# Kernel optimization log

Measured on AMD Instinct MI355X. Metric: run time of the kernel, lower is better.

## Reference

```python
import jax, jax.numpy as jnp
import numpy as np

V = 163842  # icosphere level 7: 10*4^7 + 2
K = 6       # neighbors per vertex
G = 5       # gradient directions (conv kernel_size/stride)


def setup_inputs() -> dict:
    key = jax.random.key(0)
    k1, k2, k3, k4, k5 = jax.random.split(key, 5)
    N, C_in, C_out = 2, 32, 64
    x = jax.random.normal(k1, (N, C_in, V), dtype=jnp.float32)
    neighbor_idx = jax.random.randint(k2, (V, K), 0, V, dtype=jnp.int32)
    grad_w = jax.random.normal(k3, (V, G, K), dtype=jnp.float32) * 0.1
    conv_w = jax.random.normal(k4, (C_out, C_in, G), dtype=jnp.float32) * 0.05
    conv_b = jax.random.normal(k5, (C_out,), dtype=jnp.float32) * 0.01
    return {"x": x, "neighbor_idx": neighbor_idx, "grad_w": grad_w,
            "conv_w": conv_w, "conv_b": conv_b}


def reference(x, neighbor_idx, grad_w, conv_w, conv_b):
    # x: (N, C, V); neighbor_idx: (V, K); grad_w: (V, G, K)
    # 1) icosphere gradient: gather K neighbors per vertex, weighted sum -> (N, C, V, G)
    gathered = x[:, :, neighbor_idx]                       # (N, C, V, K)
    grads = jnp.einsum('ncvk,vgk->ncvg', gathered, grad_w)  # (N, C, V, G)
    # 2) Conv1d(kernel_size=5, stride=5) on (N, C, V*G) == per-vertex contraction over (c, g)
    out = jnp.einsum('ncvg,ocg->nov', grads, conv_w) + conv_b[None, :, None]
    return out  # (N, C_out, V)
```

## Files before the change

### kernel.cpp

```cpp
#include <hip/hip_runtime.h>
#include <hip/hip_bf16.h>

#define V_   163842
#define K_   6
#define G_   5
#define N_   2
#define CIN  32
#define COUT 64
#define CG   160
#define TV   64
#define CGP  168

typedef __attribute__((ext_vector_type(8))) short bf16x8;
typedef __attribute__((ext_vector_type(4))) float f32x4;
typedef __attribute__((ext_vector_type(2))) float f32x2;

__device__ __forceinline__ float bf2f(unsigned int u16) {
  union { unsigned int u; float f; } c; c.u = u16 << 16; return c.f;
}
__device__ __forceinline__ unsigned short f2bf(float f) {
  union { float f; unsigned int u; } c; c.f = f;
  unsigned int r = c.u + 0x7fffu + ((c.u >> 16) & 1u);
  return (unsigned short)(r >> 16);
}

__global__ __launch_bounds__(256) void transpose_kernel(const float* __restrict__ x,
                                                        unsigned short* __restrict__ xt) {
  int v = blockIdx.x * 256 + threadIdx.x;
  if (v >= V_) return;
  const float* x0 = x + v;
  const float* x1 = x + (size_t)CIN * V_ + v;
  unsigned int words[CIN];
#pragma unroll
  for (int c = 0; c < CIN; ++c) {
    float a = x0[(size_t)c * V_];
    float b = x1[(size_t)c * V_];
    words[c] = (unsigned int)f2bf(a) | ((unsigned int)f2bf(b) << 16);
  }
  uint4* dst = (uint4*)(xt + (size_t)v * (2 * CIN));
#pragma unroll
  for (int i = 0; i < 8; ++i)
    dst[i] = make_uint4(words[4 * i], words[4 * i + 1], words[4 * i + 2], words[4 * i + 3]);
}

__global__ __launch_bounds__(256, 4) void icoconv_kernel(
    const unsigned short* __restrict__ xt,
    const int* __restrict__ nbr,
    const float* __restrict__ gw,
    const float* __restrict__ convw,
    const float* __restrict__ convb,
    float* __restrict__ out) {
  __shared__ int   idx_s[TV * K_];
  __shared__ float gw_s[TV * G_ * K_];
  __shared__ __align__(16) unsigned short G_s[N_][TV][CGP];

  const int t  = threadIdx.x;
  const int v0 = blockIdx.x * TV;

  for (int i = t; i < TV * K_; i += 256) {
    int gi = v0 * K_ + i;
    idx_s[i] = (gi < V_ * K_) ? nbr[gi] : 0;
  }
  __syncthreads();

  const int cp = t & 15;
  const int vb = t >> 4;
  uint2 u[4][K_];
#pragma unroll
  for (int pass = 0; pass < 4; ++pass) {
    const int vl = vb + pass * 16;
#pragma unroll
    for (int k = 0; k < K_; ++k) {
      const int j = idx_s[vl * K_ + k];
      u[pass][k] = *(const uint2*)(xt + (size_t)j * (2 * CIN) + 4 * cp);
    }
  }

  for (int i = t; i < TV * G_ * K_; i += 256) {
    int gi = v0 * G_ * K_ + i;
    gw_s[i] = (gi < V_ * G_ * K_) ? gw[gi] : 0.0f;
  }
  __syncthreads();

#pragma unroll
  for (int pass = 0; pass < 4; ++pass) {
    const int vl = vb + pass * 16;
    f32x2 acc[N_][G_];
#pragma unroll
    for (int n = 0; n < N_; ++n)
#pragma unroll
      for (int g = 0; g < G_; ++g) acc[n][g] = (f32x2){0.0f, 0.0f};

#pragma unroll
    for (int k = 0; k < K_; ++k) {
      const uint2 uu = u[pass][k];
      const f32x2 x0 = {bf2f(uu.x & 0xffffu), bf2f(uu.y & 0xffffu)};
      const f32x2 x1 = {bf2f(uu.x >> 16),     bf2f(uu.y >> 16)};
#pragma unroll
      for (int g = 0; g < G_; ++g) {
        const float w = gw_s[vl * (G_ * K_) + g * K_ + k];
        const f32x2 w2 = {w, w};
        acc[0][g] += x0 * w2;
        acc[1][g] += x1 * w2;
      }
    }
#pragma unroll
    for (int n = 0; n < N_; ++n) {
      unsigned int* dst = (unsigned int*)&G_s[n][vl][cp * 10];
      unsigned short h[10];
#pragma unroll
      for (int c01 = 0; c01 < 2; ++c01)
#pragma unroll
        for (int g = 0; g < G_; ++g) h[c01 * G_ + g] = f2bf(acc[n][g][c01]);
#pragma unroll
      for (int i = 0; i < 5; ++i)
        dst[i] = (unsigned int)h[2 * i] | ((unsigned int)h[2 * i + 1] << 16);
    }
  }
  __syncthreads();

  const int lane = t & 63;
  const int wave = t >> 6;
  const int o0   = wave * 16;
  const int row  = lane & 15;
  const int kg   = lane >> 4;

  bf16x8 afrag[5];
#pragma unroll
  for (int ks = 0; ks < 5; ++ks) {
    const float* wp = convw + (size_t)(o0 + row) * CG + ks * 32 + kg * 8;
    const float4 lo = *(const float4*)wp;
    const float4 hi = *(const float4*)(wp + 4);
    bf16x8 a;
    a[0] = (short)f2bf(lo.x); a[1] = (short)f2bf(lo.y);
    a[2] = (short)f2bf(lo.z); a[3] = (short)f2bf(lo.w);
    a[4] = (short)f2bf(hi.x); a[5] = (short)f2bf(hi.y);
    a[6] = (short)f2bf(hi.z); a[7] = (short)f2bf(hi.w);
    afrag[ks] = a;
  }
  float bias[4];
#pragma unroll
  for (int r = 0; r < 4; ++r) bias[r] = convb[o0 + kg * 4 + r];

#pragma unroll
  for (int n = 0; n < N_; ++n) {
#pragma unroll
    for (int vt = 0; vt < 4; ++vt) {
      f32x4 acc = {bias[0], bias[1], bias[2], bias[3]};
#pragma unroll
      for (int ks = 0; ks < 5; ++ks) {
        bf16x8 bfrag = *(const bf16x8*)(&G_s[n][vt * 16 + row][ks * 32 + kg * 8]);
        acc = __builtin_amdgcn_mfma_f32_16x16x32_bf16(afrag[ks], bfrag, acc, 0, 0, 0);
      }
      const int v = v0 + vt * 16 + row;
      if (v < V_) {
#pragma unroll
        for (int r = 0; r < 4; ++r)
          out[(size_t)(n * COUT + o0 + kg * 4 + r) * V_ + v] = acc[r];
      }
    }
  }
}

extern "C" void kernel_launch(void* const* d_in, const int* in_sizes, int n_in,
                              void* d_out, int out_size, void* d_ws, size_t ws_size,
                              hipStream_t stream) {
  const float* x     = (const float*)d_in[0];
  const int*   nbr   = (const int*)d_in[1];
  const float* gw    = (const float*)d_in[2];
  const float* convw = (const float*)d_in[3];
  const float* convb = (const float*)d_in[4];
  float* out = (float*)d_out;
  unsigned short* xt = (unsigned short*)d_ws;

  transpose_kernel<<<(V_ + 255) / 256, 256, 0, stream>>>(x, xt);

  const int nblk = (V_ + TV - 1) / TV;
  icoconv_kernel<<<nblk, 256, 0, stream>>>(xt, nbr, gw, convw, convb, out);
}
```

Before: 80.25 us.

## Split batch across blocks with per-batch bf16 table and nontemporal traffic

The transposed bf16 table becomes two per-batch tables, and each block now handles one vertex tile for a single batch element. Block IDs are swizzled so both batches of nearby tiles run together, which doubles the grid, halves shared memory per block and lets more blocks stay resident. Nontemporal loads and stores are used for the streamed input and output, and a sched_barrier keeps the gather loads grouped. In exchange, neighbour indices and gradient weights are loaded twice, and each gathered load is narrower (4 bytes instead of 8).

```diff
diff --git a/kernel.cpp b/kernel.cpp
--- a/kernel.cpp
+++ b/kernel.cpp
@@ -10,6 +10,8 @@
 #define CG   160
 #define TV   64
 #define CGP  168
+#define VTILES 2561
+#define GRIDX  (8 * 641)
 
 typedef __attribute__((ext_vector_type(8))) short bf16x8;
 typedef __attribute__((ext_vector_type(4))) float f32x4;
@@ -25,26 +27,28 @@
 }
 
 __global__ __launch_bounds__(256) void transpose_kernel(const float* __restrict__ x,
-                                                        unsigned short* __restrict__ xt) {
+                                                        unsigned short* __restrict__ xtn) {
   int v = blockIdx.x * 256 + threadIdx.x;
   if (v >= V_) return;
-  const float* x0 = x + v;
-  const float* x1 = x + (size_t)CIN * V_ + v;
-  unsigned int words[CIN];
 #pragma unroll
-  for (int c = 0; c < CIN; ++c) {
-    float a = x0[(size_t)c * V_];
-    float b = x1[(size_t)c * V_];
-    words[c] = (unsigned int)f2bf(a) | ((unsigned int)f2bf(b) << 16);
+  for (int n = 0; n < N_; ++n) {
+    const float* xp = x + (size_t)n * CIN * V_ + v;
+    unsigned int words[CIN / 2];
+#pragma unroll
+    for (int w = 0; w < CIN / 2; ++w) {
+      float a = __builtin_nontemporal_load(xp + (size_t)(2 * w) * V_);
+      float b = __builtin_nontemporal_load(xp + (size_t)(2 * w + 1) * V_);
+      words[w] = (unsigned int)f2bf(a) | ((unsigned int)f2bf(b) << 16);
+    }
+    uint4* dst = (uint4*)(xtn + ((size_t)n * V_ + v) * CIN);
+#pragma unroll
+    for (int i = 0; i < 4; ++i)
+      dst[i] = make_uint4(words[4 * i], words[4 * i + 1], words[4 * i + 2], words[4 * i + 3]);
   }
-  uint4* dst = (uint4*)(xt + (size_t)v * (2 * CIN));
-#pragma unroll
-  for (int i = 0; i < 8; ++i)
-    dst[i] = make_uint4(words[4 * i], words[4 * i + 1], words[4 * i + 2], words[4 * i + 3]);
 }
 
 __global__ __launch_bounds__(256, 4) void icoconv_kernel(
-    const unsigned short* __restrict__ xt,
+    const unsigned short* __restrict__ xtn,
     const int* __restrict__ nbr,
     const float* __restrict__ gw,
     const float* __restrict__ convw,
@@ -52,10 +56,15 @@
     float* __restrict__ out) {
   __shared__ int   idx_s[TV * K_];
   __shared__ float gw_s[TV * G_ * K_];
-  __shared__ __align__(16) unsigned short G_s[N_][TV][CGP];
+  __shared__ __align__(16) unsigned short G_s[TV][CGP];
 
-  const int t  = threadIdx.x;
-  const int v0 = blockIdx.x * TV;
+  const int bid   = blockIdx.x;
+  const int n     = (bid & 7) >> 2;
+  const int vtile = (bid >> 3) * 4 + (bid & 3);
+  if (vtile >= VTILES) return;
+  const int v0 = vtile * TV;
+
+  const int t = threadIdx.x;
 
   for (int i = t; i < TV * K_; i += 256) {
     int gi = v0 * K_ + i;
@@ -65,16 +74,18 @@
 
   const int cp = t & 15;
   const int vb = t >> 4;
-  uint2 u[4][K_];
+  const unsigned short* tab = xtn + (size_t)n * V_ * CIN;
+  unsigned int u[4][K_];
 #pragma unroll
   for (int pass = 0; pass < 4; ++pass) {
     const int vl = vb + pass * 16;
 #pragma unroll
     for (int k = 0; k < K_; ++k) {
       const int j = idx_s[vl * K_ + k];
-      u[pass][k] = *(const uint2*)(xt + (size_t)j * (2 * CIN) + 4 * cp);
+      u[pass][k] = *(const unsigned int*)(tab + (size_t)j * CIN + 2 * cp);
     }
   }
+  __builtin_amdgcn_sched_barrier(0);
 
   for (int i = t; i < TV * G_ * K_; i += 256) {
     int gi = v0 * G_ * K_ + i;
@@ -85,37 +96,29 @@
 #pragma unroll
   for (int pass = 0; pass < 4; ++pass) {
     const int vl = vb + pass * 16;
-    f32x2 acc[N_][G_];
+    f32x2 acc[G_];
 #pragma unroll
-    for (int n = 0; n < N_; ++n)
-#pragma unroll
-      for (int g = 0; g < G_; ++g) acc[n][g] = (f32x2){0.0f, 0.0f};
+    for (int g = 0; g < G_; ++g) acc[g] = (f32x2){0.0f, 0.0f};
 
 #pragma unroll
     for (int k = 0; k < K_; ++k) {
-      const uint2 uu = u[pass][k];
-      const f32x2 x0 = {bf2f(uu.x & 0xffffu), bf2f(uu.y & 0xffffu)};
-      const f32x2 x1 = {bf2f(uu.x >> 16),     bf2f(uu.y >> 16)};
+      const unsigned int uu = u[pass][k];
+      const f32x2 xv = {bf2f(uu & 0xffffu), bf2f(uu >> 16)};
 #pragma unroll
       for (int g = 0; g < G_; ++g) {
         const float w = gw_s[vl * (G_ * K_) + g * K_ + k];
-        const f32x2 w2 = {w, w};
-        acc[0][g] += x0 * w2;
-        acc[1][g] += x1 * w2;
+        acc[g] += xv * (f32x2){w, w};
       }
     }
+    unsigned int* dst = (unsigned int*)&G_s[vl][cp * 10];
+    unsigned short h[10];
 #pragma unroll
-    for (int n = 0; n < N_; ++n) {
-      unsigned int* dst = (unsigned int*)&G_s[n][vl][cp * 10];
-      unsigned short h[10];
+    for (int c01 = 0; c01 < 2; ++c01)
 #pragma unroll
-      for (int c01 = 0; c01 < 2; ++c01)
+      for (int g = 0; g < G_; ++g) h[c01 * G_ + g] = f2bf(acc[g][c01]);
 #pragma unroll
-        for (int g = 0; g < G_; ++g) h[c01 * G_ + g] = f2bf(acc[n][g][c01]);
-#pragma unroll
-      for (int i = 0; i < 5; ++i)
-        dst[i] = (unsigned int)h[2 * i] | ((unsigned int)h[2 * i + 1] << 16);
-    }
+    for (int i = 0; i < 5; ++i)
+      dst[i] = (unsigned int)h[2 * i] | ((unsigned int)h[2 * i + 1] << 16);
   }
   __syncthreads();
 
@@ -143,21 +146,19 @@
   for (int r = 0; r < 4; ++r) bias[r] = convb[o0 + kg * 4 + r];
 
 #pragma unroll
-  for (int n = 0; n < N_; ++n) {
+  for (int vt = 0; vt < 4; ++vt) {
+    f32x4 acc = {bias[0], bias[1], bias[2], bias[3]};
 #pragma unroll
-    for (int vt = 0; vt < 4; ++vt) {
-      f32x4 acc = {bias[0], bias[1], bias[2], bias[3]};
+    for (int ks = 0; ks < 5; ++ks) {
+      bf16x8 bfrag = *(const bf16x8*)(&G_s[vt * 16 + row][ks * 32 + kg * 8]);
+      acc = __builtin_amdgcn_mfma_f32_16x16x32_bf16(afrag[ks], bfrag, acc, 0, 0, 0);
+    }
+    const int v = v0 + vt * 16 + row;
+    if (v < V_) {
 #pragma unroll
-      for (int ks = 0; ks < 5; ++ks) {
-        bf16x8 bfrag = *(const bf16x8*)(&G_s[n][vt * 16 + row][ks * 32 + kg * 8]);
-        acc = __builtin_amdgcn_mfma_f32_16x16x32_bf16(afrag[ks], bfrag, acc, 0, 0, 0);
-      }
-      const int v = v0 + vt * 16 + row;
-      if (v < V_) {
-#pragma unroll
-        for (int r = 0; r < 4; ++r)
-          out[(size_t)(n * COUT + o0 + kg * 4 + r) * V_ + v] = acc[r];
-      }
+      for (int r = 0; r < 4; ++r)
+        __builtin_nontemporal_store(acc[r],
+            &out[(size_t)(n * COUT + o0 + kg * 4 + r) * V_ + v]);
     }
   }
 }
@@ -171,10 +172,8 @@
   const float* convw = (const float*)d_in[3];
   const float* convb = (const float*)d_in[4];
   float* out = (float*)d_out;
-  unsigned short* xt = (unsigned short*)d_ws;
+  unsigned short* xtn = (unsigned short*)d_ws;
 
-  transpose_kernel<<<(V_ + 255) / 256, 256, 0, stream>>>(x, xt);
-
-  const int nblk = (V_ + TV - 1) / TV;
-  icoconv_kernel<<<nblk, 256, 0, stream>>>(xt, nbr, gw, convw, convb, out);
+  transpose_kernel<<<(V_ + 255) / 256, 256, 0, stream>>>(x, xtn);
+  icoconv_kernel<<<GRIDX, 256, 0, stream>>>(xtn, nbr, gw, convw, convb, out);
 }
```

New measurement: 130.7 us. 1.63x slower.
